# Kernel tuning notes

Hardware: AMD Instinct MI355X
Metric: run time of the kernel (lower is better)

## Reference

```python
import jax, jax.numpy as jnp
import numpy as np

B, H, S, D = 2, 16, 2048, 64

def setup_inputs() -> dict:
    key = jax.random.key(0)
    kq, kk, kv = jax.random.split(key, 3)
    q = jax.random.normal(kq, (B, H, S, D), dtype=jnp.float32)
    k = jax.random.normal(kk, (B, H, S, D), dtype=jnp.float32)
    v = jax.random.normal(kv, (B, H, S, D), dtype=jnp.float32)
    return {"q": q, "k": k, "v": v}

def reference(q, k, v):
    # Faithful to the source: raw exp (no max-subtraction), no 1/sqrt(d) scaling.
    scores = jnp.einsum("bhsd,bhtd->bhst", q, k)          # [B,H,S,S]
    scores_exp = jnp.exp(scores)
    probs = scores_exp / jnp.sum(scores_exp, axis=-1, keepdims=True)
    return jnp.einsum("bhst,bhtd->bhsd", probs, v)         # [B,H,S,D]
```

## Files before the change

### kernel.cpp

```cpp
#include <hip/hip_runtime.h>


#define LOG2E 1.44269504088896340736f

typedef _Float16 half8 __attribute__((ext_vector_type(8)));
typedef __fp16 fp16x2 __attribute__((ext_vector_type(2)));
typedef float f32x16 __attribute__((ext_vector_type(16)));

#define BH   32
#define SEQ  2048
#define DIM  64
#define QBLK 128
#define KVB  32
#define NIT  (SEQ / (2 * KVB))

union SMem {
  struct { _Float16 K[2][KVB * DIM]; _Float16 Vt[2][DIM * KVB]; } s;
  struct { float ob[2][2][2][16 * 64]; float ml[2][2][2][64]; } c;
};

static __device__ __forceinline__ unsigned pk2(float a, float b) {
  fp16x2 h = __builtin_amdgcn_cvt_pkrtz(a, b);
  return __builtin_bit_cast(unsigned, h);
}

static __device__ __forceinline__ float xmax32(float x) {
  return fmaxf(x, __shfl_xor(x, 32));
}
static __device__ __forceinline__ float xsum32(float x) {
  return x + __shfl_xor(x, 32);
}

__launch_bounds__(256, 2)
__global__ void attn_fwd(const float* __restrict__ Q, const float* __restrict__ K,
                         const float* __restrict__ V, float* __restrict__ O) {
  __shared__ __align__(16) SMem sm;

  const int tid  = threadIdx.x;
  const int lane = tid & 63;
  const int wave = tid >> 6;
  const int wq   = wave & 1;
  const int wk   = wave >> 1;
  const int hi   = lane >> 5;
  const int lq   = lane & 31;
  const bool hb  = (hi != 0);

  const int bid  = blockIdx.x;
  const int xcd  = bid & 7;
  const int slot = bid >> 3;
  const int bh   = xcd + 8 * (slot >> 4);
  const int qt   = slot & 15;

  const size_t base = (size_t)bh * SEQ * DIM;
  const int qr0 = qt * QBLK + wq * 64 + lq;
  const float* qpA = Q + base + (size_t)qr0 * DIM;
  const float* qpB = qpA + 32 * DIM;

  half8 qfA[4], qfB[4];
#pragma unroll
  for (int c = 0; c < 4; ++c) {
    float4 a0 = *(const float4*)(qpA + 16 * c + 8 * hi);
    float4 a1 = *(const float4*)(qpA + 16 * c + 8 * hi + 4);
    union { unsigned u[4]; half8 v; } h;
    h.u[0] = pk2(a0.x, a0.y); h.u[1] = pk2(a0.z, a0.w);
    h.u[2] = pk2(a1.x, a1.y); h.u[3] = pk2(a1.z, a1.w);
    qfA[c] = h.v;
    float4 b0 = *(const float4*)(qpB + 16 * c + 8 * hi);
    float4 b1 = *(const float4*)(qpB + 16 * c + 8 * hi + 4);
    h.u[0] = pk2(b0.x, b0.y); h.u[1] = pk2(b0.z, b0.w);
    h.u[2] = pk2(b1.x, b1.y); h.u[3] = pk2(b1.z, b1.w);
    qfB[c] = h.v;
  }

  f32x16 oA0 = {}, oA1 = {}, oB0 = {}, oB1 = {};
  float mA = -1e30f, lA = 0.f, mB = -1e30f, lB = 0.f;

  float4 kreg[2][2];
  float  vreg[2][8];
  const int kr  = tid >> 3;
  const int kd  = (tid & 7) * 8;
  const int vd  = tid & 63;
  const int vk0 = (tid >> 6) * 8;
  const float* kbp = K + base;
  const float* vbp = V + base;

  auto LOADT = [&](int it) {
#pragma unroll
    for (int p = 0; p < 2; ++p) {
      const int t = 2 * it + p;
      const float* kp = kbp + (size_t)(t * KVB + kr) * DIM + kd;
      kreg[p][0] = *(const float4*)(kp);
      kreg[p][1] = *(const float4*)(kp + 4);
      const float* vp = vbp + (size_t)(t * KVB + vk0) * DIM + vd;
#pragma unroll
      for (int j = 0; j < 8; ++j) vreg[p][j] = vp[j * DIM];
    }
  };

  auto STORET = [&]() {
#pragma unroll
    for (int p = 0; p < 2; ++p) {
      union { unsigned u[4]; half8 v; } h;
      h.u[0] = pk2(kreg[p][0].x, kreg[p][0].y);
      h.u[1] = pk2(kreg[p][0].z, kreg[p][0].w);
      h.u[2] = pk2(kreg[p][1].x, kreg[p][1].y);
      h.u[3] = pk2(kreg[p][1].z, kreg[p][1].w);
      const int idx = (kr * DIM + kd) ^ ((kr & 7) << 3);
      *(half8*)&sm.s.K[p][idx] = h.v;
      union { unsigned u[4]; half8 v; } g;
      g.u[0] = pk2(vreg[p][0], vreg[p][1]);
      g.u[1] = pk2(vreg[p][2], vreg[p][3]);
      g.u[2] = pk2(vreg[p][4], vreg[p][5]);
      g.u[3] = pk2(vreg[p][6], vreg[p][7]);
      const int vidx = (vd * KVB + vk0) ^ ((vd & 7) << 3);
      *(half8*)&sm.s.Vt[p][vidx] = g.v;
    }
  };

  auto softmax_set = [&](const f32x16& s, float& m, float& l,
                         f32x16& o0, f32x16& o1, half8& pv0, half8& pv1) {
    float x0 = fmaxf(fmaxf(s[0], s[1]), fmaxf(s[2], s[3]));
    float x1 = fmaxf(fmaxf(s[4], s[5]), fmaxf(s[6], s[7]));
    float x2 = fmaxf(fmaxf(s[8], s[9]), fmaxf(s[10], s[11]));
    float x3 = fmaxf(fmaxf(s[12], s[13]), fmaxf(s[14], s[15]));
    float t = xmax32(fmaxf(fmaxf(x0, x1), fmaxf(x2, x3)));
    if (__any(t > m + 8.f)) {
      const float mn = fmaxf(m, t);
      const float corr = __builtin_amdgcn_exp2f((m - mn) * LOG2E);
      m = mn; l *= corr;
#pragma unroll
      for (int i = 0; i < 16; ++i) { o0[i] *= corr; o1[i] *= corr; }
    }
    const float nml2 = -m * LOG2E;
    float p[16];
#pragma unroll
    for (int i = 0; i < 16; ++i)
      p[i] = __builtin_amdgcn_exp2f(__builtin_fmaf(s[i], LOG2E, nml2));
    float t0 = (p[0] + p[1]) + (p[2] + p[3]);
    float t1 = (p[4] + p[5]) + (p[6] + p[7]);
    float t2 = (p[8] + p[9]) + (p[10] + p[11]);
    float t3 = (p[12] + p[13]) + (p[14] + p[15]);
    l += xsum32((t0 + t1) + (t2 + t3));

    unsigned w[8];
#pragma unroll
    for (int i = 0; i < 8; ++i) w[i] = pk2(p[2 * i], p[2 * i + 1]);
    unsigned y0 = hb ? w[0] : w[2];  unsigned r0 = (unsigned)__shfl_xor((int)y0, 32);
    unsigned y1 = hb ? w[1] : w[3];  unsigned r1 = (unsigned)__shfl_xor((int)y1, 32);
    unsigned y2 = hb ? w[4] : w[6];  unsigned r2 = (unsigned)__shfl_xor((int)y2, 32);
    unsigned y3 = hb ? w[5] : w[7];  unsigned r3 = (unsigned)__shfl_xor((int)y3, 32);
    union { unsigned u[4]; half8 v; } f;
    f.u[0] = hb ? r0 : w[0];
    f.u[1] = hb ? r1 : w[1];
    f.u[2] = hb ? w[2] : r0;
    f.u[3] = hb ? w[3] : r1;
    pv0 = f.v;
    f.u[0] = hb ? r2 : w[4];
    f.u[1] = hb ? r3 : w[5];
    f.u[2] = hb ? w[6] : r2;
    f.u[3] = hb ? w[7] : r3;
    pv1 = f.v;
  };

  LOADT(0);
  for (int it = 0; it < NIT; ++it) {
    __syncthreads();
    STORET();
    if (it + 1 < NIT) LOADT(it + 1);
    __syncthreads();

    const _Float16* Kt = sm.s.K[wk];
    const _Float16* Vt = sm.s.Vt[wk];

    const int ksw = (lq & 7) << 3;
    f32x16 sA = {}, sB = {};
    __builtin_amdgcn_s_setprio(1);
#pragma unroll
    for (int c = 0; c < 4; ++c) {
      half8 a = *(const half8*)&Kt[(lq * DIM + c * 16 + hi * 8) ^ ksw];
      sA = __builtin_amdgcn_mfma_f32_32x32x16_f16(a, qfA[c], sA, 0, 0, 0);
      sB = __builtin_amdgcn_mfma_f32_32x32x16_f16(a, qfB[c], sB, 0, 0, 0);
    }
    __builtin_amdgcn_s_setprio(0);

    half8 pA0, pA1, pB0, pB1;
    softmax_set(sA, mA, lA, oA0, oA1, pA0, pA1);
    softmax_set(sB, mB, lB, oB0, oB1, pB0, pB1);

    const int d0 = lq, d1 = 32 + lq;
    const int sz0 = (d0 & 7) << 3, sz1 = (d1 & 7) << 3;
    __builtin_amdgcn_s_setprio(1);
    {
      half8 a = *(const half8*)&Vt[(d0 * KVB + 0 + hi * 8) ^ sz0];
      oA0 = __builtin_amdgcn_mfma_f32_32x32x16_f16(a, pA0, oA0, 0, 0, 0);
      oB0 = __builtin_amdgcn_mfma_f32_32x32x16_f16(a, pB0, oB0, 0, 0, 0);
    }
    {
      half8 a = *(const half8*)&Vt[(d1 * KVB + 0 + hi * 8) ^ sz1];
      oA1 = __builtin_amdgcn_mfma_f32_32x32x16_f16(a, pA0, oA1, 0, 0, 0);
      oB1 = __builtin_amdgcn_mfma_f32_32x32x16_f16(a, pB0, oB1, 0, 0, 0);
    }
    {
      half8 a = *(const half8*)&Vt[(d0 * KVB + 16 + hi * 8) ^ sz0];
      oA0 = __builtin_amdgcn_mfma_f32_32x32x16_f16(a, pA1, oA0, 0, 0, 0);
      oB0 = __builtin_amdgcn_mfma_f32_32x32x16_f16(a, pB1, oB0, 0, 0, 0);
    }
    {
      half8 a = *(const half8*)&Vt[(d1 * KVB + 16 + hi * 8) ^ sz1];
      oA1 = __builtin_amdgcn_mfma_f32_32x32x16_f16(a, pA1, oA1, 0, 0, 0);
      oB1 = __builtin_amdgcn_mfma_f32_32x32x16_f16(a, pB1, oB1, 0, 0, 0);
    }
    __builtin_amdgcn_s_setprio(0);
  }

  __syncthreads();
  if (wk == 1) {
#pragma unroll
    for (int r = 0; r < 16; ++r) {
      sm.c.ob[wq][0][0][r * 64 + lane] = oA0[r];
      sm.c.ob[wq][0][1][r * 64 + lane] = oA1[r];
      sm.c.ob[wq][1][0][r * 64 + lane] = oB0[r];
      sm.c.ob[wq][1][1][r * 64 + lane] = oB1[r];
    }
    sm.c.ml[wq][0][0][lane] = mA; sm.c.ml[wq][0][1][lane] = lA;
    sm.c.ml[wq][1][0][lane] = mB; sm.c.ml[wq][1][1][lane] = lB;
  }
  __syncthreads();
  if (wk == 0) {
    auto emit = [&](int set, int qrow, const f32x16& o0, const f32x16& o1,
                    float m, float l) {
      const float mb = sm.c.ml[wq][set][0][lane];
      const float lb = sm.c.ml[wq][set][1][lane];
      const float mx = fmaxf(m, mb);
      const float ca = __builtin_amdgcn_exp2f((m - mx) * LOG2E);
      const float cb = __builtin_amdgcn_exp2f((mb - mx) * LOG2E);
      const float inv = 1.0f / (l * ca + lb * cb);
      float* op = O + base + (size_t)qrow * DIM;
#pragma unroll
      for (int g = 0; g < 4; ++g) {
        float4 r0, r1;
        r0.x = (o0[4*g+0] * ca + sm.c.ob[wq][set][0][(4*g+0)*64 + lane] * cb) * inv;
        r0.y = (o0[4*g+1] * ca + sm.c.ob[wq][set][0][(4*g+1)*64 + lane] * cb) * inv;
        r0.z = (o0[4*g+2] * ca + sm.c.ob[wq][set][0][(4*g+2)*64 + lane] * cb) * inv;
        r0.w = (o0[4*g+3] * ca + sm.c.ob[wq][set][0][(4*g+3)*64 + lane] * cb) * inv;
        r1.x = (o1[4*g+0] * ca + sm.c.ob[wq][set][1][(4*g+0)*64 + lane] * cb) * inv;
        r1.y = (o1[4*g+1] * ca + sm.c.ob[wq][set][1][(4*g+1)*64 + lane] * cb) * inv;
        r1.z = (o1[4*g+2] * ca + sm.c.ob[wq][set][1][(4*g+2)*64 + lane] * cb) * inv;
        r1.w = (o1[4*g+3] * ca + sm.c.ob[wq][set][1][(4*g+3)*64 + lane] * cb) * inv;
        *(float4*)(op + 8 * g + 4 * hi) = r0;
        *(float4*)(op + 32 + 8 * g + 4 * hi) = r1;
      }
    };
    emit(0, qr0,      oA0, oA1, mA, lA);
    emit(1, qr0 + 32, oB0, oB1, mB, lB);
  }
}

extern "C" void kernel_launch(void* const* d_in, const int* in_sizes, int n_in,
                              void* d_out, int out_size, void* d_ws, size_t ws_size,
                              hipStream_t stream) {
  const float* q = (const float*)d_in[0];
  const float* k = (const float*)d_in[1];
  const float* v = (const float*)d_in[2];
  float* o = (float*)d_out;
  attn_fwd<<<BH * (SEQ / QBLK), 256, 0, stream>>>(q, k, v, o);
}
```

Measured before the change: 67.35 us.

## Split KV range across four waves with 64-query blocks and tree merge

```diff
diff --git a/kernel.cpp b/kernel.cpp
--- a/kernel.cpp
+++ b/kernel.cpp
@@ -10,13 +10,14 @@
 #define BH   32
 #define SEQ  2048
 #define DIM  64
-#define QBLK 128
+#define QBLK 64
 #define KVB  32
-#define NIT  (SEQ / (2 * KVB))
+#define NPAR 4
+#define NIT  (SEQ / (NPAR * KVB))
 
 union SMem {
-  struct { _Float16 K[2][KVB * DIM]; _Float16 Vt[2][DIM * KVB]; } s;
-  struct { float ob[2][2][2][16 * 64]; float ml[2][2][2][64]; } c;
+  struct { _Float16 K[NPAR][KVB * DIM]; _Float16 Vt[NPAR][DIM * KVB]; } s;
+  struct { float ob[2][4][16 * 64]; float ml[2][4][64]; } c;
 };
 
 static __device__ __forceinline__ unsigned pk2(float a, float b) {
@@ -31,16 +32,14 @@
   return x + __shfl_xor(x, 32);
 }
 
-__launch_bounds__(256, 2)
+__launch_bounds__(256, 3)
 __global__ void attn_fwd(const float* __restrict__ Q, const float* __restrict__ K,
                          const float* __restrict__ V, float* __restrict__ O) {
   __shared__ __align__(16) SMem sm;
 
   const int tid  = threadIdx.x;
   const int lane = tid & 63;
-  const int wave = tid >> 6;
-  const int wq   = wave & 1;
-  const int wk   = wave >> 1;
+  const int wk   = tid >> 6;
   const int hi   = lane >> 5;
   const int lq   = lane & 31;
   const bool hb  = (hi != 0);
@@ -48,11 +47,11 @@
   const int bid  = blockIdx.x;
   const int xcd  = bid & 7;
   const int slot = bid >> 3;
-  const int bh   = xcd + 8 * (slot >> 4);
-  const int qt   = slot & 15;
+  const int bh   = xcd + 8 * (slot >> 5);
+  const int qt   = slot & 31;
 
   const size_t base = (size_t)bh * SEQ * DIM;
-  const int qr0 = qt * QBLK + wq * 64 + lq;
+  const int qr0 = qt * QBLK + lq;
   const float* qpA = Q + base + (size_t)qr0 * DIM;
   const float* qpB = qpA + 32 * DIM;
 
@@ -75,8 +74,8 @@
   f32x16 oA0 = {}, oA1 = {}, oB0 = {}, oB1 = {};
   float mA = -1e30f, lA = 0.f, mB = -1e30f, lB = 0.f;
 
-  float4 kreg[2][2];
-  float  vreg[2][8];
+  float4 kreg[NPAR][2];
+  float  vreg[NPAR][8];
   const int kr  = tid >> 3;
   const int kd  = (tid & 7) * 8;
   const int vd  = tid & 63;
@@ -86,8 +85,8 @@
 
   auto LOADT = [&](int it) {
 #pragma unroll
-    for (int p = 0; p < 2; ++p) {
-      const int t = 2 * it + p;
+    for (int p = 0; p < NPAR; ++p) {
+      const int t = NPAR * it + p;
       const float* kp = kbp + (size_t)(t * KVB + kr) * DIM + kd;
       kreg[p][0] = *(const float4*)(kp);
       kreg[p][1] = *(const float4*)(kp + 4);
@@ -99,7 +98,7 @@
 
   auto STORET = [&]() {
 #pragma unroll
-    for (int p = 0; p < 2; ++p) {
+    for (int p = 0; p < NPAR; ++p) {
       union { unsigned u[4]; half8 v; } h;
       h.u[0] = pk2(kreg[p][0].x, kreg[p][0].y);
       h.u[1] = pk2(kreg[p][0].z, kreg[p][0].w);
@@ -213,46 +212,75 @@
     __builtin_amdgcn_s_setprio(0);
   }
 
-  __syncthreads();
-  if (wk == 1) {
+  auto publish = [&](int s) {
 #pragma unroll
     for (int r = 0; r < 16; ++r) {
-      sm.c.ob[wq][0][0][r * 64 + lane] = oA0[r];
-      sm.c.ob[wq][0][1][r * 64 + lane] = oA1[r];
-      sm.c.ob[wq][1][0][r * 64 + lane] = oB0[r];
-      sm.c.ob[wq][1][1][r * 64 + lane] = oB1[r];
-    }
-    sm.c.ml[wq][0][0][lane] = mA; sm.c.ml[wq][0][1][lane] = lA;
-    sm.c.ml[wq][1][0][lane] = mB; sm.c.ml[wq][1][1][lane] = lB;
-  }
+      sm.c.ob[s][0][r * 64 + lane] = oA0[r];
+      sm.c.ob[s][1][r * 64 + lane] = oA1[r];
+      sm.c.ob[s][2][r * 64 + lane] = oB0[r];
+      sm.c.ob[s][3][r * 64 + lane] = oB1[r];
+    }
+    sm.c.ml[s][0][lane] = mA; sm.c.ml[s][1][lane] = lA;
+    sm.c.ml[s][2][lane] = mB; sm.c.ml[s][3][lane] = lB;
+  };
+  auto merge = [&](int s) {
+    {
+      const float mb = sm.c.ml[s][0][lane], lb = sm.c.ml[s][1][lane];
+      const float mx = fmaxf(mA, mb);
+      const float ca = __builtin_amdgcn_exp2f((mA - mx) * LOG2E);
+      const float cb = __builtin_amdgcn_exp2f((mb - mx) * LOG2E);
+#pragma unroll
+      for (int r = 0; r < 16; ++r) {
+        oA0[r] = oA0[r] * ca + sm.c.ob[s][0][r * 64 + lane] * cb;
+        oA1[r] = oA1[r] * ca + sm.c.ob[s][1][r * 64 + lane] * cb;
+      }
+      lA = lA * ca + lb * cb; mA = mx;
+    }
+    {
+      const float mb = sm.c.ml[s][2][lane], lb = sm.c.ml[s][3][lane];
+      const float mx = fmaxf(mB, mb);
+      const float ca = __builtin_amdgcn_exp2f((mB - mx) * LOG2E);
+      const float cb = __builtin_amdgcn_exp2f((mb - mx) * LOG2E);
+#pragma unroll
+      for (int r = 0; r < 16; ++r) {
+        oB0[r] = oB0[r] * ca + sm.c.ob[s][2][r * 64 + lane] * cb;
+        oB1[r] = oB1[r] * ca + sm.c.ob[s][3][r * 64 + lane] * cb;
+      }
+      lB = lB * ca + lb * cb; mB = mx;
+    }
+  };
+
+  __syncthreads();
+  if (wk == 1) publish(0);
+  if (wk == 3) publish(1);
+  __syncthreads();
+  if (wk == 0) merge(0);
+  if (wk == 2) merge(1);
+  __syncthreads();
+  if (wk == 2) publish(0);
   __syncthreads();
   if (wk == 0) {
-    auto emit = [&](int set, int qrow, const f32x16& o0, const f32x16& o1,
-                    float m, float l) {
-      const float mb = sm.c.ml[wq][set][0][lane];
-      const float lb = sm.c.ml[wq][set][1][lane];
-      const float mx = fmaxf(m, mb);
-      const float ca = __builtin_amdgcn_exp2f((m - mx) * LOG2E);
-      const float cb = __builtin_amdgcn_exp2f((mb - mx) * LOG2E);
-      const float inv = 1.0f / (l * ca + lb * cb);
-      float* op = O + base + (size_t)qrow * DIM;
-#pragma unroll
-      for (int g = 0; g < 4; ++g) {
-        float4 r0, r1;
-        r0.x = (o0[4*g+0] * ca + sm.c.ob[wq][set][0][(4*g+0)*64 + lane] * cb) * inv;
-        r0.y = (o0[4*g+1] * ca + sm.c.ob[wq][set][0][(4*g+1)*64 + lane] * cb) * inv;
-        r0.z = (o0[4*g+2] * ca + sm.c.ob[wq][set][0][(4*g+2)*64 + lane] * cb) * inv;
-        r0.w = (o0[4*g+3] * ca + sm.c.ob[wq][set][0][(4*g+3)*64 + lane] * cb) * inv;
-        r1.x = (o1[4*g+0] * ca + sm.c.ob[wq][set][1][(4*g+0)*64 + lane] * cb) * inv;
-        r1.y = (o1[4*g+1] * ca + sm.c.ob[wq][set][1][(4*g+1)*64 + lane] * cb) * inv;
-        r1.z = (o1[4*g+2] * ca + sm.c.ob[wq][set][1][(4*g+2)*64 + lane] * cb) * inv;
-        r1.w = (o1[4*g+3] * ca + sm.c.ob[wq][set][1][(4*g+3)*64 + lane] * cb) * inv;
-        *(float4*)(op + 8 * g + 4 * hi) = r0;
-        *(float4*)(op + 32 + 8 * g + 4 * hi) = r1;
-      }
-    };
-    emit(0, qr0,      oA0, oA1, mA, lA);
-    emit(1, qr0 + 32, oB0, oB1, mB, lB);
+    merge(0);
+    const float invA = 1.0f / lA;
+    const float invB = 1.0f / lB;
+    float* opA = O + base + (size_t)qr0 * DIM;
+    float* opB = opA + 32 * DIM;
+#pragma unroll
+    for (int g = 0; g < 4; ++g) {
+      float4 r0, r1;
+      r0.x = oA0[4*g+0] * invA; r0.y = oA0[4*g+1] * invA;
+      r0.z = oA0[4*g+2] * invA; r0.w = oA0[4*g+3] * invA;
+      r1.x = oA1[4*g+0] * invA; r1.y = oA1[4*g+1] * invA;
+      r1.z = oA1[4*g+2] * invA; r1.w = oA1[4*g+3] * invA;
+      *(float4*)(opA + 8 * g + 4 * hi) = r0;
+      *(float4*)(opA + 32 + 8 * g + 4 * hi) = r1;
+      r0.x = oB0[4*g+0] * invB; r0.y = oB0[4*g+1] * invB;
+      r0.z = oB0[4*g+2] * invB; r0.w = oB0[4*g+3] * invB;
+      r1.x = oB1[4*g+0] * invB; r1.y = oB1[4*g+1] * invB;
+      r1.z = oB1[4*g+2] * invB; r1.w = oB1[4*g+3] * invB;
+      *(float4*)(opB + 8 * g + 4 * hi) = r0;
+      *(float4*)(opB + 32 + 8 * g + 4 * hi) = r1;
+    }
   }
 }
 
```

Result: slower. 232.2 us (+244.7%).
